# Kernel optimization log

Hardware: AMD Instinct MI355X
Metric: run time of the kernel (lower is better)

Reference implementation:

```python
import jax, jax.numpy as jnp
import numpy as np

B, F, N, P, G = 256, 100, 512, 512, 10  # trials, time bins, units, channels, sessions
SCALE = 1.0


def setup_inputs() -> dict:
    key = jax.random.key(0)
    k = jax.random.split(key, 6)
    x = jax.random.normal(k[0], (B, F, N), dtype=jnp.float32)
    eid = jax.random.randint(k[1], (B,), 0, G, dtype=jnp.int32)
    # Per-session stitcher Linear(N -> 2N) and projector Linear(2N -> P)
    W1 = jax.random.normal(k[2], (G, N, 2 * N), dtype=jnp.float32) / np.sqrt(N)
    b1 = jax.random.normal(k[3], (G, 2 * N), dtype=jnp.float32) * 0.01
    W2 = jax.random.normal(k[4], (G, 2 * N, P), dtype=jnp.float32) / np.sqrt(2 * N)
    b2 = jax.random.normal(k[5], (G, P), dtype=jnp.float32) * 0.01
    return {"x": x, "eid": eid, "W1": W1, "b1": b1, "W2": W2, "b2": b2}


def reference(x, eid, W1, b1, W2, b2):
    # Equivalent to the per-eid gather -> Linear -> Softsign*scale -> Linear -> scatter,
    # expressed as batched GEMMs with per-sample gathered weights (same math, vectorized).
    h = jnp.einsum('bfn,bnm->bfm', x, W1[eid]) + b1[eid][:, None, :]   # [B, F, 2N]
    h = (h / (1.0 + jnp.abs(h))) * SCALE                               # Softsign * scale
    out = jnp.einsum('bfm,bmp->bfp', h, W2[eid]) + b2[eid][:, None, :]  # [B, F, P]
    return out
```

## Files before the change

### kernel.cpp

```cpp
#include <hip/hip_runtime.h>
#include <hip/hip_bf16.h>
#include <cstdint>

typedef __attribute__((ext_vector_type(8))) short short8;
typedef __attribute__((ext_vector_type(8))) unsigned short ushort8;
typedef __attribute__((ext_vector_type(4))) float f32x4;

#define B_TRIALS 256
#define F_BINS   100
#define N_UNITS  512
#define P_CH     512
#define G_SESS   10
#define H_DIM    1024
#define TOT_ROWS (B_TRIALS * F_BINS)
#define NT_PAD   216

#define PREP_CASTX_BLOCKS 2048
#define PREP_W1_BLOCKS    5120
#define PREP_W2_BLOCKS    5120
#define PREP_TOTAL (1 + PREP_CASTX_BLOCKS + PREP_W1_BLOCKS + PREP_W2_BLOCKS)

__device__ __forceinline__ unsigned short f2bf(float f) {
  unsigned int u = __builtin_bit_cast(unsigned int, f);
  u += 0x7fffu + ((u >> 16) & 1u);
  return (unsigned short)(u >> 16);
}

__device__ __forceinline__ void gload16(const void* gsrc, void* ldst) {
  __builtin_amdgcn_global_load_lds(
      (const __attribute__((address_space(1))) unsigned int*)gsrc,
      (__attribute__((address_space(3))) unsigned int*)ldst, 16, 0, 0);
}

__device__ __forceinline__ void transpose_tile(const float* __restrict__ src,
                                               unsigned short* __restrict__ dst,
                                               int K, int N, int g, int n0, int k0,
                                               float (*tile)[33]) {
  const float* s = src + (size_t)g * K * N;
  unsigned short* d = dst + (size_t)g * N * K;
  int t = threadIdx.x;
  int r = t >> 3, c = (t & 7) * 4;
  float4 v = *(const float4*)(s + (size_t)(k0 + r) * N + n0 + c);
  tile[r][c + 0] = v.x; tile[r][c + 1] = v.y;
  tile[r][c + 2] = v.z; tile[r][c + 3] = v.w;
  __syncthreads();
  ushort4 o;
  o.x = f2bf(tile[c + 0][r]);
  o.y = f2bf(tile[c + 1][r]);
  o.z = f2bf(tile[c + 2][r]);
  o.w = f2bf(tile[c + 3][r]);
  *(ushort4*)(d + (size_t)(n0 + r) * K + k0 + c) = o;
}

__global__ void prep(const float* __restrict__ x, const int* __restrict__ eid,
                     const float* __restrict__ W1, const float* __restrict__ W2,
                     unsigned short* __restrict__ xb,
                     unsigned short* __restrict__ W1t,
                     unsigned short* __restrict__ W2t,
                     int* __restrict__ rowmap, int* __restrict__ tile_meta) {
  __shared__ float tile[32][33];
  __shared__ int e[B_TRIALS], cnt[G_SESS], off[G_SESS], groff[G_SESS + 1], perm[B_TRIALS];
  const int bid = blockIdx.x;
  const int t = threadIdx.x;

  if (bid == 0) {
    e[t] = eid[t];
    if (t < G_SESS) cnt[t] = 0;
    __syncthreads();
    atomicAdd(&cnt[e[t]], 1);
    __syncthreads();
    if (t == 0) {
      int s = 0, r = 0;
      for (int g = 0; g < G_SESS; g++) {
        off[g] = s; s += cnt[g];
        groff[g] = r; r += cnt[g] * F_BINS;
      }
      groff[G_SESS] = r;
    }
    __syncthreads();
    int g = e[t], rank = 0;
    for (int j = 0; j < t; j++) rank += (e[j] == g);
    perm[off[g] + rank] = t;
    __syncthreads();
    for (int i = t; i < TOT_ROWS; i += 256) {
      int gg = 0;
      while (gg + 1 < G_SESS && i >= groff[gg + 1]) gg++;
      int loc = i - groff[gg];
      rowmap[i] = perm[off[gg] + loc / F_BINS] * F_BINS + loc % F_BINS;
    }
    if (t == 0) {
      int ti = 0;
      for (int g2 = 0; g2 < G_SESS; g2++) {
        int rows = cnt[g2] * F_BINS;
        int base = groff[g2];
        for (int r0 = 0; r0 < rows; r0 += 128) {
          tile_meta[ti * 3 + 0] = g2;
          tile_meta[ti * 3 + 1] = base + r0;
          tile_meta[ti * 3 + 2] = (rows - r0 < 128) ? (rows - r0) : 128;
          ti++;
        }
      }
      for (; ti < NT_PAD; ti++) {
        tile_meta[ti * 3 + 0] = -1; tile_meta[ti * 3 + 1] = 0; tile_meta[ti * 3 + 2] = 0;
      }
    }
  } else if (bid <= PREP_CASTX_BLOCKS) {
    const int n8 = B_TRIALS * F_BINS * N_UNITS / 8;
    int i = (bid - 1) * 256 + t;
    const int stride = PREP_CASTX_BLOCKS * 256;
    for (; i < n8; i += stride) {
      float4 v0 = ((const float4*)x)[(size_t)i * 2];
      float4 v1 = ((const float4*)x)[(size_t)i * 2 + 1];
      ushort8 w;
      w[0] = f2bf(v0.x); w[1] = f2bf(v0.y); w[2] = f2bf(v0.z); w[3] = f2bf(v0.w);
      w[4] = f2bf(v1.x); w[5] = f2bf(v1.y); w[6] = f2bf(v1.z); w[7] = f2bf(v1.w);
      ((ushort8*)xb)[i] = w;
    }
  } else if (bid <= PREP_CASTX_BLOCKS + PREP_W1_BLOCKS) {
    int tt = bid - 1 - PREP_CASTX_BLOCKS;
    int n0 = (tt & 31) * 32, k0 = ((tt >> 5) & 15) * 32, g = tt >> 9;
    transpose_tile(W1, W1t, N_UNITS, H_DIM, g, n0, k0, tile);
  } else {
    int tt = bid - 1 - PREP_CASTX_BLOCKS - PREP_W1_BLOCKS;
    int n0 = (tt & 15) * 32, k0 = ((tt >> 4) & 31) * 32, g = tt >> 9;
    transpose_tile(W2, W2t, H_DIM, P_CH, g, n0, k0, tile);
  }
}


template<int KTOT, int NOUT, int NC, bool IS2>
__global__ __launch_bounds__(256, 2) void gemm_grouped(
    const unsigned short* __restrict__ Asrc,
    const unsigned short* __restrict__ Wt,
    const float* __restrict__ bias,
    const int* __restrict__ rowmap,
    const int* __restrict__ tile_meta,
    unsigned short* __restrict__ hout,
    float* __restrict__ out) {
  __shared__ __align__(16) unsigned short Ash[2][128 * 64];
  __shared__ __align__(16) unsigned short Bsh[2][128 * 64];

  const int wg = blockIdx.x;
  const int xcd = wg & 7, slot = wg >> 3;
  const int mt = xcd * (NT_PAD / 8) + slot / NC;
  const int nc = slot % NC;

  const int g = tile_meta[mt * 3 + 0];
  if (g < 0) return;
  const int row0 = tile_meta[mt * 3 + 1];
  const int valid = tile_meta[mt * 3 + 2];
  const int ncol0 = nc * 128;

  const int tid = threadIdx.x;
  const int lane = tid & 63;
  const int w = tid >> 6;
  const int wm = w >> 1, wn = w & 1;
  const int lr = lane & 15, lq = lane >> 4;

  const unsigned short* Wg = Wt + (size_t)g * NOUT * KTOT + (size_t)ncol0 * KTOT;
  const unsigned short* aptr[4];
  const unsigned short* bptr[4];
  {
    int rbase = tid >> 3, q = tid & 7;
#pragma unroll
    for (int it = 0; it < 4; it++) {
      int row = it * 32 + rbase;
      int ks = (q ^ (row & 7)) * 8;
      int grow = row0 + row; if (grow > TOT_ROWS - 1) grow = TOT_ROWS - 1;
      int sr = IS2 ? grow : rowmap[grow];
      aptr[it] = Asrc + (size_t)sr * KTOT + ks;
      bptr[it] = Wg + (size_t)row * KTOT + ks;
    }
  }

#define STAGE(kt, buf) do {                                                  \
    size_t _ko = (size_t)(kt) * 64;                                          \
    _Pragma("unroll")                                                        \
    for (int _it = 0; _it < 4; _it++) {                                      \
      gload16(aptr[_it] + _ko, &Ash[buf][(_it * 256 + (tid & 192)) * 8]);    \
      gload16(bptr[_it] + _ko, &Bsh[buf][(_it * 256 + (tid & 192)) * 8]);    \
    }                                                                        \
  } while (0)

  f32x4 acc[4][4];
#pragma unroll
  for (int m = 0; m < 4; m++)
#pragma unroll
    for (int n = 0; n < 4; n++) acc[m][n] = (f32x4){0.f, 0.f, 0.f, 0.f};

  constexpr int NK = KTOT / 64;

  STAGE(0, 0);
  __syncthreads();

  for (int t = 0; t < NK; ++t) {
    const int cur = t & 1;
    if (t + 1 < NK) STAGE(t + 1, cur ^ 1);

    const unsigned short* Ap = &Ash[cur][0];
    const unsigned short* Bp = &Bsh[cur][0];
    __builtin_amdgcn_s_setprio(1);
#pragma unroll
    for (int kk = 0; kk < 2; kk++) {
      int kslot = kk * 4 + lq;
      short8 av[4], bv[4];
#pragma unroll
      for (int m = 0; m < 4; m++) {
        int row = wm * 64 + m * 16 + lr;
        av[m] = *(const short8*)&Ap[row * 64 + ((kslot ^ (row & 7)) * 8)];
      }
#pragma unroll
      for (int n = 0; n < 4; n++) {
        int col = wn * 64 + n * 16 + lr;
        bv[n] = *(const short8*)&Bp[col * 64 + ((kslot ^ (col & 7)) * 8)];
      }
#pragma unroll
      for (int n = 0; n < 4; n++)
#pragma unroll
        for (int m = 0; m < 4; m++)
          acc[m][n] = __builtin_amdgcn_mfma_f32_16x16x32_bf16(av[m], bv[n], acc[m][n], 0, 0, 0);
    }
    __builtin_amdgcn_s_setprio(0);
    __syncthreads();
  }

  float bv4[4];
#pragma unroll
  for (int n = 0; n < 4; n++)
    bv4[n] = bias[(size_t)g * NOUT + ncol0 + wn * 64 + n * 16 + lr];

  if (!IS2) {
#pragma unroll
    for (int m = 0; m < 4; m++)
#pragma unroll
      for (int r4 = 0; r4 < 4; r4++) {
        int lrow = wm * 64 + m * 16 + lq * 4 + r4;
        if (lrow < valid) {
          size_t base = (size_t)(row0 + lrow) * H_DIM + ncol0 + wn * 64 + lr;
#pragma unroll
          for (int n = 0; n < 4; n++) {
            float v = acc[m][n][r4] + bv4[n];
            v = v / (1.0f + fabsf(v));
            hout[base + n * 16] = f2bf(v);
          }
        }
      }
  } else {
#pragma unroll
    for (int m = 0; m < 4; m++)
#pragma unroll
      for (int r4 = 0; r4 < 4; r4++) {
        int lrow = wm * 64 + m * 16 + lq * 4 + r4;
        if (lrow < valid) {
          int orow = rowmap[row0 + lrow];
          size_t base = (size_t)orow * P_CH + ncol0 + wn * 64 + lr;
#pragma unroll
          for (int n = 0; n < 4; n++)
            out[base + n * 16] = acc[m][n][r4] + bv4[n];
        }
      }
  }
#undef STAGE
}

extern "C" void kernel_launch(void* const* d_in, const int* in_sizes, int n_in,
                              void* d_out, int out_size, void* d_ws, size_t ws_size,
                              hipStream_t stream) {
  const float* x  = (const float*)d_in[0];
  const int* eid  = (const int*)d_in[1];
  const float* W1 = (const float*)d_in[2];
  const float* b1 = (const float*)d_in[3];
  const float* W2 = (const float*)d_in[4];
  const float* b2 = (const float*)d_in[5];
  float* out = (float*)d_out;

  unsigned short* W1t = (unsigned short*)d_ws;
  unsigned short* W2t = W1t + (size_t)G_SESS * H_DIM * N_UNITS;
  unsigned short* h   = W2t + (size_t)G_SESS * P_CH * H_DIM;
  int* rowmap    = (int*)(h + (size_t)TOT_ROWS * H_DIM);
  int* tile_meta = rowmap + TOT_ROWS;
  unsigned short* xb = (unsigned short*)d_out;

  prep<<<PREP_TOTAL, 256, 0, stream>>>(x, eid, W1, W2, xb, W1t, W2t, rowmap, tile_meta);
  gemm_grouped<N_UNITS, H_DIM, 8, false><<<NT_PAD * 8, 256, 0, stream>>>(
      xb, W1t, b1, rowmap, tile_meta, h, out);
  gemm_grouped<H_DIM, P_CH, 4, true><<<NT_PAD * 4, 256, 0, stream>>>(
      h, W2t, b2, rowmap, tile_meta, h, out);
}
```

Baseline: 130.4 us.

## Replace LDS double buffering with single buffer and raise occupancy to 4 blocks

The grouped GEMM drops its double-buffered LDS staging for a single 32 KB buffer. Each k-step now loads its tile, waits for the loads and syncs before computing, and the launch-bounds occupancy hint goes from 2 to 4 blocks per CU. The s_setprio hints are also removed. The aim is to hide memory latency through more resident waves instead of in-block prefetch, at the cost of serialising load and compute within each block and adding a barrier per iteration.

Result: faster. 116.2 us (-10.9%).

```diff
diff --git a/kernel.cpp b/kernel.cpp
--- a/kernel.cpp
+++ b/kernel.cpp
@@ -129,7 +129,7 @@
 
 
 template<int KTOT, int NOUT, int NC, bool IS2>
-__global__ __launch_bounds__(256, 2) void gemm_grouped(
+__global__ __launch_bounds__(256, 4) void gemm_grouped(
     const unsigned short* __restrict__ Asrc,
     const unsigned short* __restrict__ Wt,
     const float* __restrict__ bias,
@@ -137,8 +137,8 @@
     const int* __restrict__ tile_meta,
     unsigned short* __restrict__ hout,
     float* __restrict__ out) {
-  __shared__ __align__(16) unsigned short Ash[2][128 * 64];
-  __shared__ __align__(16) unsigned short Bsh[2][128 * 64];
+  __shared__ __align__(16) unsigned short Ash[128 * 64];
+  __shared__ __align__(16) unsigned short Bsh[128 * 64];
 
   const int wg = blockIdx.x;
   const int xcd = wg & 7, slot = wg >> 3;
@@ -173,15 +173,6 @@
     }
   }
 
-#define STAGE(kt, buf) do {                                                  \
-    size_t _ko = (size_t)(kt) * 64;                                          \
-    _Pragma("unroll")                                                        \
-    for (int _it = 0; _it < 4; _it++) {                                      \
-      gload16(aptr[_it] + _ko, &Ash[buf][(_it * 256 + (tid & 192)) * 8]);    \
-      gload16(bptr[_it] + _ko, &Bsh[buf][(_it * 256 + (tid & 192)) * 8]);    \
-    }                                                                        \
-  } while (0)
-
   f32x4 acc[4][4];
 #pragma unroll
   for (int m = 0; m < 4; m++)
@@ -190,16 +181,17 @@
 
   constexpr int NK = KTOT / 64;
 
-  STAGE(0, 0);
-  __syncthreads();
-
   for (int t = 0; t < NK; ++t) {
-    const int cur = t & 1;
-    if (t + 1 < NK) STAGE(t + 1, cur ^ 1);
-
-    const unsigned short* Ap = &Ash[cur][0];
-    const unsigned short* Bp = &Bsh[cur][0];
-    __builtin_amdgcn_s_setprio(1);
+    const size_t ko = (size_t)t * 64;
+    __syncthreads();
+#pragma unroll
+    for (int it = 0; it < 4; it++) {
+      gload16(aptr[it] + ko, &Ash[(it * 256 + (tid & 192)) * 8]);
+      gload16(bptr[it] + ko, &Bsh[(it * 256 + (tid & 192)) * 8]);
+    }
+    asm volatile("s_waitcnt vmcnt(0) lgkmcnt(0)" ::: "memory");
+    __syncthreads();
+
 #pragma unroll
     for (int kk = 0; kk < 2; kk++) {
       int kslot = kk * 4 + lq;
@@ -207,12 +199,12 @@
 #pragma unroll
       for (int m = 0; m < 4; m++) {
         int row = wm * 64 + m * 16 + lr;
-        av[m] = *(const short8*)&Ap[row * 64 + ((kslot ^ (row & 7)) * 8)];
+        av[m] = *(const short8*)&Ash[row * 64 + ((kslot ^ (row & 7)) * 8)];
       }
 #pragma unroll
       for (int n = 0; n < 4; n++) {
         int col = wn * 64 + n * 16 + lr;
-        bv[n] = *(const short8*)&Bp[col * 64 + ((kslot ^ (col & 7)) * 8)];
+        bv[n] = *(const short8*)&Bsh[col * 64 + ((kslot ^ (col & 7)) * 8)];
       }
 #pragma unroll
       for (int n = 0; n < 4; n++)
@@ -220,8 +212,6 @@
         for (int m = 0; m < 4; m++)
           acc[m][n] = __builtin_amdgcn_mfma_f32_16x16x32_bf16(av[m], bv[n], acc[m][n], 0, 0, 0);
     }
-    __builtin_amdgcn_s_setprio(0);
-    __syncthreads();
   }
 
   float bv4[4];
@@ -260,7 +250,6 @@
         }
       }
   }
-#undef STAGE
 }
 
 extern "C" void kernel_launch(void* const* d_in, const int* in_sizes, int n_in,
```
